# Performance work log

Hardware: AMD Instinct MI355X
Metric: run time of the kernel (lower is better)

## Reference

```python
import jax, jax.numpy as jnp
import numpy as np

N, T, E, D, U = 32, 2048, 512, 1024, 256


def setup_inputs() -> dict:
    key = jax.random.key(0)
    ks = jax.random.split(key, 6)
    queries = jax.random.normal(ks[0], (N, 1, D), dtype=jnp.float32)
    prev = jax.random.uniform(ks[1], (N, T), dtype=jnp.float32)
    prev = prev / jnp.sum(prev, axis=1, keepdims=True)  # distribution-like initial alignment
    memory = jax.random.normal(ks[2], (N, T, E), dtype=jnp.float32)
    W_q = jax.random.normal(ks[3], (D, U), dtype=jnp.float32) * (1.0 / np.sqrt(D))
    W_k = jax.random.normal(ks[4], (E, U), dtype=jnp.float32) * (1.0 / np.sqrt(E))
    v = jax.random.uniform(ks[5], (U,), dtype=jnp.float32)
    return {"queries": queries, "previous_alignments": prev, "memory": memory,
            "W_q": W_q, "W_k": W_k, "v": v}


def safe_cumprod_exclusive(x):
    # exclusive cumprod via log-space cumsum, clamped like the torch original
    logsum = jnp.cumsum(jnp.log(jnp.clip(x, 1e-20, 1.0)), axis=1)  # [N,T]
    excl = jnp.concatenate([jnp.zeros_like(logsum[:, :1]), logsum], axis=1)[:, :-1]
    return jnp.exp(excl)


def reference(queries, previous_alignments, memory, W_q, W_k, v):
    # Bahdanau additive score (normalize=False path)
    proj_key = jnp.einsum('bte,eu->btu', memory, W_k)          # set_memory
    proj_q = jnp.einsum('bqd,du->bqu', queries, W_q)           # [N,1,U]
    weights = jnp.einsum('btu,u->bt', jnp.tanh(proj_q + proj_key), v)  # [N,T]
    p_choose = jax.nn.sigmoid(weights)
    # monotonic attention recursion in cumsum/cumprod form
    cumprod_1mp = safe_cumprod_exclusive(1.0 - p_choose)
    alignments = p_choose * cumprod_1mp * jnp.cumsum(
        previous_alignments / jnp.clip(cumprod_1mp, 1e-10, 1.0), axis=1)
    contexts = jnp.einsum('bt,bte->be', alignments, memory)    # bmm + squeeze
    return (contexts, alignments)
```

## Files before the change

kernel.cpp:

```cpp
#include <hip/hip_runtime.h>
#include <math.h>

#define N_ 32
#define T_ 2048
#define E_ 512
#define D_ 1024
#define U_ 256

typedef __attribute__((ext_vector_type(8))) short bf16x8;
typedef __attribute__((ext_vector_type(16))) float f32x16;

__device__ __forceinline__ short f2bf_rne(float x) {
  unsigned int u = __float_as_uint(x);
  unsigned int r = u + 0x7FFFu + ((u >> 16) & 1u);
  return (short)(r >> 16);
}
__device__ __forceinline__ short f2bf_trunc(float x) {
  return (short)(__float_as_uint(x) >> 16);
}
__device__ __forceinline__ float bf2f(short h) {
  return __uint_as_float(((unsigned int)(unsigned short)h) << 16);
}
__device__ __forceinline__ float fast_tanh(float x) {
  float t = exp2f(x * 2.8853900817779268f);
  return 1.0f - 2.0f * __builtin_amdgcn_rcpf(t + 1.0f);
}
__device__ __forceinline__ float fast_sigmoid(float w) {
  return __builtin_amdgcn_rcpf(1.0f + exp2f(-1.4426950408889634f * w));
}

__global__ __launch_bounds__(256) void prep_kernel(
    const float* __restrict__ Wk, const float* __restrict__ queries,
    const float* __restrict__ Wq, bf16x8* __restrict__ whiP,
    bf16x8* __restrict__ wloP, float* __restrict__ pq_part) {
  const int wg = blockIdx.x, tid = threadIdx.x;
  if (wg < 64) {
    const int fid = wg * 256 + tid;
    const int lane = fid & 63;
    const int ub = (fid >> 6) & 7;
    const int kc = (fid >> 9) & 3;
    const int c = fid >> 11;
    const int u = ub * 32 + (lane & 31);
    const int e0 = c * 64 + kc * 16 + (lane >> 5) * 8;
    bf16x8 H, L;
#pragma unroll
    for (int j = 0; j < 8; ++j) {
      float x = Wk[(size_t)(e0 + j) * U_ + u];
      short h = f2bf_trunc(x);
      H[j] = h;
      L[j] = f2bf_rne(x - bf2f(h));
    }
    whiP[fid] = H;
    wloP[fid] = L;
  } else {
    const int ch = (wg - 64) & 3;
    const int bb = (wg - 64) >> 2;
    const int d0 = ch * 256;
    const float* q = queries + bb * D_ + d0;
    const float* wq = Wq + (size_t)d0 * U_ + tid;
    float acc = 0.f;
#pragma unroll 8
    for (int d = 0; d < 256; ++d)
      acc = fmaf(q[d], wq[(size_t)d * U_], acc);
    pq_part[(bb * 4 + ch) * U_ + tid] = acc;
  }
}

__global__ __launch_bounds__(256, 3) void score_kernel(
    const float* __restrict__ memory, const bf16x8* __restrict__ whiP,
    const bf16x8* __restrict__ wloP, const float* __restrict__ pq_part,
    const float* __restrict__ v, float* __restrict__ p_choose) {
  __shared__ short sA[2][64 * 64];
  __shared__ float smem_w[4][64];

  const int b = blockIdx.y;
  const int t0 = blockIdx.x * 64;
  const int tid = threadIdx.x;
  const int lane = tid & 63;
  const int ty = tid >> 6;
  const int l31 = lane & 31;
  const int half = lane >> 5;

  f32x16 acc[2][2];
#pragma unroll
  for (int mt = 0; mt < 2; ++mt)
#pragma unroll
    for (int nt = 0; nt < 2; ++nt)
#pragma unroll
      for (int r = 0; r < 16; ++r) acc[mt][nt][r] = 0.f;

  const int sr = tid >> 2;
  const int cs = (tid & 3) * 8;
  const int s0 = tid & 3;
  const int sw = sr & 7;
  const float* srow = memory + ((size_t)(b * T_ + t0 + sr)) * E_ + cs;
  char* const bp0 = (char*)&sA[0][0] + sr * 128;
  char* const bp1 = (char*)&sA[1][0] + sr * 128;

  float4 xr[2];
#pragma unroll
  for (int j = 0; j < 2; ++j) xr[j] = *(const float4*)(srow + j * 4);

  auto do_stage = [&](char* bp) {
    float xs[8] = {xr[0].x, xr[0].y, xr[0].z, xr[0].w,
                   xr[1].x, xr[1].y, xr[1].z, xr[1].w};
    bf16x8 H, L;
#pragma unroll
    for (int i = 0; i < 8; ++i) {
      short h = f2bf_trunc(xs[i]);
      H[i] = h;
      L[i] = f2bf_rne(xs[i] - bf2f(h));
    }
    *(bf16x8*)(bp + ((s0 ^ sw) * 16)) = H;
    *(bf16x8*)(bp + (((s0 + 4) ^ sw) * 16)) = L;
  };

  do_stage(bp0);
  __syncthreads();

  int cur = 0;
  for (int it = 0; it < 16; ++it) {
    if (it < 15) {
      const float* src = srow + (it + 1) * 32;
#pragma unroll
      for (int j = 0; j < 2; ++j) xr[j] = *(const float4*)(src + j * 4);
    }
    const char* base = (const char*)&sA[cur][0];
#pragma unroll
    for (int kc = 0; kc < 2; ++kc) {
      bf16x8 bh[2], bl[2];
#pragma unroll
      for (int nt = 0; nt < 2; ++nt) {
        const int fidx = ((it * 2 + kc) * 8 + (ty * 2 + nt)) * 64 + lane;
        bh[nt] = whiP[fidx];
        bl[nt] = wloP[fidx];
      }
      const int sl = kc * 2 + half;
      bf16x8 ah[2], al[2];
#pragma unroll
      for (int mt = 0; mt < 2; ++mt) {
        const int m = mt * 32 + l31;
        ah[mt] = *(const bf16x8*)(base + (size_t)m * 128 + ((sl ^ (m & 7)) * 16));
        al[mt] = *(const bf16x8*)(base + (size_t)m * 128 + (((sl + 4) ^ (m & 7)) * 16));
      }
#pragma unroll
      for (int mt = 0; mt < 2; ++mt)
#pragma unroll
        for (int nt = 0; nt < 2; ++nt) {
          acc[mt][nt] = __builtin_amdgcn_mfma_f32_32x32x16_bf16(ah[mt], bh[nt], acc[mt][nt], 0, 0, 0);
          acc[mt][nt] = __builtin_amdgcn_mfma_f32_32x32x16_bf16(ah[mt], bl[nt], acc[mt][nt], 0, 0, 0);
          acc[mt][nt] = __builtin_amdgcn_mfma_f32_32x32x16_bf16(al[mt], bh[nt], acc[mt][nt], 0, 0, 0);
        }
    }
    if (it < 15) do_stage(cur ? bp0 : bp1);
    __syncthreads();
    cur ^= 1;
  }

  const int u0 = ty * 64 + l31;
  const int u1 = u0 + 32;
  float pq0 = 0.f, pq1 = 0.f;
#pragma unroll
  for (int c = 0; c < 4; ++c) {
    pq0 += pq_part[(b * 4 + c) * U_ + u0];
    pq1 += pq_part[(b * 4 + c) * U_ + u1];
  }
  const float v0 = v[u0], v1 = v[u1];
#pragma unroll
  for (int mt = 0; mt < 2; ++mt)
#pragma unroll
    for (int r = 0; r < 16; ++r) {
      float s = fast_tanh(acc[mt][0][r] + pq0) * v0 + fast_tanh(acc[mt][1][r] + pq1) * v1;
#pragma unroll
      for (int off = 1; off < 32; off <<= 1) s += __shfl_xor(s, off, 64);
      if (l31 == 0) {
        const int row = mt * 32 + (r & 3) + 8 * (r >> 2) + 4 * half;
        smem_w[ty][row] = s;
      }
    }
  __syncthreads();
  if (tid < 64) {
    const float w = smem_w[0][tid] + smem_w[1][tid] + smem_w[2][tid] + smem_w[3][tid];
    p_choose[b * T_ + t0 + tid] = fast_sigmoid(w);
  }
}

__device__ __forceinline__ float block_incl_scan(float val, float* sbuf, int tid) {
  float x = val;
  sbuf[tid] = x;
  __syncthreads();
#pragma unroll
  for (int off = 1; off < 256; off <<= 1) {
    float t = (tid >= off) ? sbuf[tid - off] : 0.f;
    __syncthreads();
    x += t;
    sbuf[tid] = x;
    __syncthreads();
  }
  return x;
}

__global__ __launch_bounds__(256) void scan_kernel(
    const float* __restrict__ p_choose, const float* __restrict__ prev,
    float* __restrict__ align_out, float* __restrict__ ctx_out) {
  __shared__ float sbuf[256];
  const int b = blockIdx.x, tid = threadIdx.x;
  ctx_out[b * E_ + tid] = 0.f;
  ctx_out[b * E_ + 256 + tid] = 0.f;
  const int base = b * T_ + tid * 8;
  float4 p0 = *(const float4*)(p_choose + base);
  float4 p1 = *(const float4*)(p_choose + base + 4);
  float p[8] = {p0.x, p0.y, p0.z, p0.w, p1.x, p1.y, p1.z, p1.w};
  float s[8];
  float run = 0.f;
#pragma unroll
  for (int k = 0; k < 8; ++k) {
    float x = 1.0f - p[k];
    x = fminf(fmaxf(x, 1e-20f), 1.0f);
    run += logf(x);
    s[k] = run;
  }
  float incl = block_incl_scan(run, sbuf, tid);
  float excl = incl - run;
  float cp[8];
#pragma unroll
  for (int k = 0; k < 8; ++k)
    cp[k] = expf(excl + (k ? s[k - 1] : 0.f));
  float4 r0 = *(const float4*)(prev + base);
  float4 r1 = *(const float4*)(prev + base + 4);
  float pr[8] = {r0.x, r0.y, r0.z, r0.w, r1.x, r1.y, r1.z, r1.w};
  float s2[8];
  float run2 = 0.f;
#pragma unroll
  for (int k = 0; k < 8; ++k) {
    float d = fminf(fmaxf(cp[k], 1e-10f), 1.0f);
    run2 += pr[k] / d;
    s2[k] = run2;
  }
  float incl2 = block_incl_scan(run2, sbuf, tid);
  float excl2 = incl2 - run2;
#pragma unroll
  for (int k = 0; k < 8; ++k)
    p[k] = p[k] * cp[k] * (excl2 + s2[k]);
  *(float4*)(align_out + base) = make_float4(p[0], p[1], p[2], p[3]);
  *(float4*)(align_out + base + 4) = make_float4(p[4], p[5], p[6], p[7]);
}

__global__ __launch_bounds__(256) void ctx_kernel(
    const float* __restrict__ memory, const float* __restrict__ align,
    float* __restrict__ ctx_out) {
  const int wg = blockIdx.x, tid = threadIdx.x;
  const int b = wg >> 4;
  const int t0 = (wg & 15) * 128 + (tid >> 7) * 64;
  const int col = (tid & 127) * 4;
  const float* mrow = memory + ((size_t)(b * T_ + t0)) * E_ + col;
  const float* arow = align + b * T_ + t0;
  float4 a = make_float4(0.f, 0.f, 0.f, 0.f);
  for (int t = 0; t < 64; t += 4) {
    float4 m0 = *(const float4*)(mrow + (size_t)(t + 0) * E_);
    float4 m1 = *(const float4*)(mrow + (size_t)(t + 1) * E_);
    float4 m2 = *(const float4*)(mrow + (size_t)(t + 2) * E_);
    float4 m3 = *(const float4*)(mrow + (size_t)(t + 3) * E_);
    float a0 = arow[t], a1 = arow[t + 1], a2 = arow[t + 2], a3 = arow[t + 3];
    a.x = fmaf(a0, m0.x, a.x); a.y = fmaf(a0, m0.y, a.y);
    a.z = fmaf(a0, m0.z, a.z); a.w = fmaf(a0, m0.w, a.w);
    a.x = fmaf(a1, m1.x, a.x); a.y = fmaf(a1, m1.y, a.y);
    a.z = fmaf(a1, m1.z, a.z); a.w = fmaf(a1, m1.w, a.w);
    a.x = fmaf(a2, m2.x, a.x); a.y = fmaf(a2, m2.y, a.y);
    a.z = fmaf(a2, m2.z, a.z); a.w = fmaf(a2, m2.w, a.w);
    a.x = fmaf(a3, m3.x, a.x); a.y = fmaf(a3, m3.y, a.y);
    a.z = fmaf(a3, m3.z, a.z); a.w = fmaf(a3, m3.w, a.w);
  }
  float* dst = ctx_out + b * E_ + col;
  atomicAdd(dst + 0, a.x);
  atomicAdd(dst + 1, a.y);
  atomicAdd(dst + 2, a.z);
  atomicAdd(dst + 3, a.w);
}

extern "C" void kernel_launch(void* const* d_in, const int* in_sizes, int n_in,
                              void* d_out, int out_size, void* d_ws, size_t ws_size,
                              hipStream_t stream) {
  (void)in_sizes; (void)n_in; (void)out_size; (void)ws_size;
  const float* queries = (const float*)d_in[0];
  const float* prev    = (const float*)d_in[1];
  const float* memory  = (const float*)d_in[2];
  const float* Wq      = (const float*)d_in[3];
  const float* Wk      = (const float*)d_in[4];
  const float* v       = (const float*)d_in[5];

  float* out = (float*)d_out;
  float* ctx_out = out;
  float* align_out = out + N_ * E_;

  float* ws = (float*)d_ws;
  bf16x8* whiP    = (bf16x8*)ws;
  bf16x8* wloP    = (bf16x8*)(ws + 65536);
  float* p_choose = ws + 131072;
  float* pq_part  = ws + 196608;

  prep_kernel<<<dim3(64 + 128), 256, 0, stream>>>(Wk, queries, Wq, whiP, wloP, pq_part);
  score_kernel<<<dim3(T_ / 64, N_), 256, 0, stream>>>(memory, whiP, wloP, pq_part, v, p_choose);
  scan_kernel<<<dim3(N_), 256, 0, stream>>>(p_choose, prev, align_out, ctx_out);
  ctx_kernel<<<dim3(512), 256, 0, stream>>>(memory, align_out, ctx_out);
}
```

Before: 281.3 us.

## Enlarge score tile to 128 rows with per-wave private staging buffers

The score kernel now handles 128 time steps per block, using a 2x2 wave layout: each wave covers 64 rows and 128 units and stages its own 64-row slice of memory into a private double-buffered LDS region. This removes the per-iteration block-wide barriers and halves how often each W_k fragment is reloaded per time row. The cost is more accumulators and staging registers per thread, lower occupancy (launch bound 2), four times the LDS, and half as many blocks in the grid.

Measured after the change: 282.3 us. About the same (+0.3%).

```diff
diff --git a/kernel.cpp b/kernel.cpp
--- a/kernel.cpp
+++ b/kernel.cpp
@@ -66,74 +66,71 @@
   }
 }
 
-__global__ __launch_bounds__(256, 3) void score_kernel(
+__global__ __launch_bounds__(256, 2) void score_kernel(
     const float* __restrict__ memory, const bf16x8* __restrict__ whiP,
     const bf16x8* __restrict__ wloP, const float* __restrict__ pq_part,
     const float* __restrict__ v, float* __restrict__ p_choose) {
-  __shared__ short sA[2][64 * 64];
-  __shared__ float smem_w[4][64];
+  __shared__ short sA[4][2][64 * 64];
+  __shared__ float smem_w[2][128];
 
   const int b = blockIdx.y;
-  const int t0 = blockIdx.x * 64;
+  const int t0 = blockIdx.x * 128;
   const int tid = threadIdx.x;
   const int lane = tid & 63;
-  const int ty = tid >> 6;
+  const int w = tid >> 6;
+  const int rw = w >> 1;
+  const int uw = w & 1;
   const int l31 = lane & 31;
   const int half = lane >> 5;
 
-  f32x16 acc[2][2];
+  f32x16 acc[2][4];
 #pragma unroll
   for (int mt = 0; mt < 2; ++mt)
 #pragma unroll
-    for (int nt = 0; nt < 2; ++nt)
-#pragma unroll
-      for (int r = 0; r < 16; ++r) acc[mt][nt][r] = 0.f;
-
-  const int sr = tid >> 2;
-  const int cs = (tid & 3) * 8;
-  const int s0 = tid & 3;
-  const int sw = sr & 7;
-  const float* srow = memory + ((size_t)(b * T_ + t0 + sr)) * E_ + cs;
-  char* const bp0 = (char*)&sA[0][0] + sr * 128;
-  char* const bp1 = (char*)&sA[1][0] + sr * 128;
-
-  float4 xr[2];
-#pragma unroll
-  for (int j = 0; j < 2; ++j) xr[j] = *(const float4*)(srow + j * 4);
+    for (int nb = 0; nb < 4; ++nb)
+#pragma unroll
+      for (int r = 0; r < 16; ++r) acc[mt][nb][r] = 0.f;
+
+  const int tr0 = t0 + rw * 64;
+  const float* srow = memory + ((size_t)(b * T_ + tr0 + lane)) * E_;
+  char* const bpw = (char*)&sA[w][0][0] + lane * 128;
+  const int sw = lane & 7;
+
+  float4 xr[8];
 
   auto do_stage = [&](char* bp) {
-    float xs[8] = {xr[0].x, xr[0].y, xr[0].z, xr[0].w,
-                   xr[1].x, xr[1].y, xr[1].z, xr[1].w};
-    bf16x8 H, L;
-#pragma unroll
-    for (int i = 0; i < 8; ++i) {
-      short h = f2bf_trunc(xs[i]);
-      H[i] = h;
-      L[i] = f2bf_rne(xs[i] - bf2f(h));
-    }
-    *(bf16x8*)(bp + ((s0 ^ sw) * 16)) = H;
-    *(bf16x8*)(bp + (((s0 + 4) ^ sw) * 16)) = L;
+#pragma unroll
+    for (int c = 0; c < 4; ++c) {
+      float xs[8] = {xr[2 * c].x, xr[2 * c].y, xr[2 * c].z, xr[2 * c].w,
+                     xr[2 * c + 1].x, xr[2 * c + 1].y, xr[2 * c + 1].z, xr[2 * c + 1].w};
+      bf16x8 H, L;
+#pragma unroll
+      for (int i = 0; i < 8; ++i) {
+        short h = f2bf_trunc(xs[i]);
+        H[i] = h;
+        L[i] = f2bf_rne(xs[i] - bf2f(h));
+      }
+      *(bf16x8*)(bp + ((c ^ sw) * 16)) = H;
+      *(bf16x8*)(bp + (((c + 4) ^ sw) * 16)) = L;
+    }
   };
 
-  do_stage(bp0);
-  __syncthreads();
-
-  int cur = 0;
+#pragma unroll
+  for (int j = 0; j < 8; ++j) xr[j] = *(const float4*)(srow + j * 4);
+  do_stage(bpw);
+#pragma unroll
+  for (int j = 0; j < 8; ++j) xr[j] = *(const float4*)(srow + 32 + j * 4);
+
   for (int it = 0; it < 16; ++it) {
-    if (it < 15) {
-      const float* src = srow + (it + 1) * 32;
-#pragma unroll
-      for (int j = 0; j < 2; ++j) xr[j] = *(const float4*)(src + j * 4);
-    }
-    const char* base = (const char*)&sA[cur][0];
+    const char* base = (const char*)&sA[w][it & 1][0];
 #pragma unroll
     for (int kc = 0; kc < 2; ++kc) {
-      bf16x8 bh[2], bl[2];
-#pragma unroll
-      for (int nt = 0; nt < 2; ++nt) {
-        const int fidx = ((it * 2 + kc) * 8 + (ty * 2 + nt)) * 64 + lane;
-        bh[nt] = whiP[fidx];
-        bl[nt] = wloP[fidx];
+      bf16x8 bh[4], bl[4];
+#pragma unroll
+      for (int nb = 0; nb < 4; ++nb) {
+        const int fidx = ((it * 2 + kc) * 8 + (uw * 4 + nb)) * 64 + lane;
+        bh[nb] = whiP[fidx];
+        bl[nb] = wloP[fidx];
       }
       const int sl = kc * 2 + half;
       bf16x8 ah[2], al[2];
@@ -146,42 +143,49 @@
 #pragma unroll
       for (int mt = 0; mt < 2; ++mt)
 #pragma unroll
-        for (int nt = 0; nt < 2; ++nt) {
-          acc[mt][nt] = __builtin_amdgcn_mfma_f32_32x32x16_bf16(ah[mt], bh[nt], acc[mt][nt], 0, 0, 0);
-          acc[mt][nt] = __builtin_amdgcn_mfma_f32_32x32x16_bf16(ah[mt], bl[nt], acc[mt][nt], 0, 0, 0);
-          acc[mt][nt] = __builtin_amdgcn_mfma_f32_32x32x16_bf16(al[mt], bh[nt], acc[mt][nt], 0, 0, 0);
+        for (int nb = 0; nb < 4; ++nb) {
+          acc[mt][nb] = __builtin_amdgcn_mfma_f32_32x32x16_bf16(ah[mt], bh[nb], acc[mt][nb], 0, 0, 0);
+          acc[mt][nb] = __builtin_amdgcn_mfma_f32_32x32x16_bf16(ah[mt], bl[nb], acc[mt][nb], 0, 0, 0);
+          acc[mt][nb] = __builtin_amdgcn_mfma_f32_32x32x16_bf16(al[mt], bh[nb], acc[mt][nb], 0, 0, 0);
         }
     }
-    if (it < 15) do_stage(cur ? bp0 : bp1);
-    __syncthreads();
-    cur ^= 1;
-  }
-
-  const int u0 = ty * 64 + l31;
-  const int u1 = u0 + 32;
-  float pq0 = 0.f, pq1 = 0.f;
-#pragma unroll
-  for (int c = 0; c < 4; ++c) {
-    pq0 += pq_part[(b * 4 + c) * U_ + u0];
-    pq1 += pq_part[(b * 4 + c) * U_ + u1];
-  }
-  const float v0 = v[u0], v1 = v[u1];
+    if (it < 15) do_stage(bpw + ((it + 1) & 1) * (64 * 128));
+    if (it < 14) {
+      const float* src = srow + (it + 2) * 32;
+#pragma unroll
+      for (int j = 0; j < 8; ++j) xr[j] = *(const float4*)(src + j * 4);
+    }
+  }
+
+  float pq[4], vv[4];
+#pragma unroll
+  for (int nb = 0; nb < 4; ++nb) {
+    const int u = uw * 128 + nb * 32 + l31;
+    float s = 0.f;
+#pragma unroll
+    for (int c = 0; c < 4; ++c) s += pq_part[(b * 4 + c) * U_ + u];
+    pq[nb] = s;
+    vv[nb] = v[u];
+  }
 #pragma unroll
   for (int mt = 0; mt < 2; ++mt)
 #pragma unroll
     for (int r = 0; r < 16; ++r) {
-      float s = fast_tanh(acc[mt][0][r] + pq0) * v0 + fast_tanh(acc[mt][1][r] + pq1) * v1;
+      float s = 0.f;
+#pragma unroll
+      for (int nb = 0; nb < 4; ++nb)
+        s += fast_tanh(acc[mt][nb][r] + pq[nb]) * vv[nb];
 #pragma unroll
       for (int off = 1; off < 32; off <<= 1) s += __shfl_xor(s, off, 64);
       if (l31 == 0) {
-        const int row = mt * 32 + (r & 3) + 8 * (r >> 2) + 4 * half;
-        smem_w[ty][row] = s;
+        const int row = rw * 64 + mt * 32 + (r & 3) + 8 * (r >> 2) + 4 * half;
+        smem_w[uw][row] = s;
       }
     }
   __syncthreads();
-  if (tid < 64) {
-    const float w = smem_w[0][tid] + smem_w[1][tid] + smem_w[2][tid] + smem_w[3][tid];
-    p_choose[b * T_ + t0 + tid] = fast_sigmoid(w);
+  if (tid < 128) {
+    const float wsum = smem_w[0][tid] + smem_w[1][tid];
+    p_choose[b * T_ + t0 + tid] = fast_sigmoid(wsum);
   }
 }
 
@@ -300,7 +304,7 @@
   float* pq_part  = ws + 196608;
 
   prep_kernel<<<dim3(64 + 128), 256, 0, stream>>>(Wk, queries, Wq, whiP, wloP, pq_part);
-  score_kernel<<<dim3(T_ / 64, N_), 256, 0, stream>>>(memory, whiP, wloP, pq_part, v, p_choose);
+  score_kernel<<<dim3(T_ / 128, N_), 256, 0, stream>>>(memory, whiP, wloP, pq_part, v, p_choose);
   scan_kernel<<<dim3(N_), 256, 0, stream>>>(p_choose, prev, align_out, ctx_out);
   ctx_kernel<<<dim3(512), 256, 0, stream>>>(memory, align_out, ctx_out);
 }
```
